# Performance work log

Measured on AMD Instinct MI355X. Metric: run time of the kernel, lower is better.

Reference implementation:

```python
import jax, jax.numpy as jnp
import numpy as np

N_USER = 250_000
N_ITEM = 250_000
E = 500_000
IN, H, C = 128, 64, 2
NEG_SLOPE = 0.01  # torch F.leaky_relu default


def setup_inputs() -> dict:
    key = jax.random.key(0)
    ks = jax.random.split(key, 24)
    d = {}
    d["feat_user"] = jax.random.normal(ks[0], (N_USER, IN), jnp.float32)
    d["feat_item"] = jax.random.normal(ks[1], (N_ITEM, IN), jnp.float32)
    # per-etype linear params, layer 1 (in_feats -> h_dim)
    s1 = 1.0 / np.sqrt(IN)
    d["W1_follows"] = jax.random.normal(ks[2], (IN, H), jnp.float32) * s1
    d["b1_follows"] = jax.random.normal(ks[3], (H,), jnp.float32) * s1
    d["W1_clicks"]  = jax.random.normal(ks[4], (IN, H), jnp.float32) * s1
    d["b1_clicks"]  = jax.random.normal(ks[5], (H,), jnp.float32) * s1
    d["W1_rev"]     = jax.random.normal(ks[6], (IN, H), jnp.float32) * s1
    d["b1_rev"]     = jax.random.normal(ks[7], (H,), jnp.float32) * s1
    # per-etype linear params, layer 2 (h_dim -> num_classes)
    s2 = 1.0 / np.sqrt(H)
    d["W2_follows"] = jax.random.normal(ks[8], (H, C), jnp.float32) * s2
    d["b2_follows"] = jax.random.normal(ks[9], (C,), jnp.float32) * s2
    d["W2_clicks"]  = jax.random.normal(ks[10], (H, C), jnp.float32) * s2
    d["b2_clicks"]  = jax.random.normal(ks[11], (C,), jnp.float32) * s2
    d["W2_rev"]     = jax.random.normal(ks[12], (H, C), jnp.float32) * s2
    d["b2_rev"]     = jax.random.normal(ks[13], (C,), jnp.float32) * s2
    # edge lists: (src, dst) per canonical etype
    d["follows_src"] = jax.random.randint(ks[14], (E,), 0, N_USER, jnp.int32)  # user->user
    d["follows_dst"] = jax.random.randint(ks[15], (E,), 0, N_USER, jnp.int32)
    d["clicks_src"]  = jax.random.randint(ks[16], (E,), 0, N_USER, jnp.int32)  # user->item
    d["clicks_dst"]  = jax.random.randint(ks[17], (E,), 0, N_ITEM, jnp.int32)
    d["rev_src"]     = jax.random.randint(ks[18], (E,), 0, N_ITEM, jnp.int32)  # item->user
    d["rev_dst"]     = jax.random.randint(ks[19], (E,), 0, N_USER, jnp.int32)
    return d


def _mean_agg(Wh, src, dst, n_dst):
    # copy_u + mean: gather transformed src feats per edge, segment-mean onto dst
    m = Wh[src]                                                   # [E, d]
    s = jax.ops.segment_sum(m, dst, num_segments=n_dst)           # [n_dst, d]
    deg = jax.ops.segment_sum(jnp.ones_like(dst, Wh.dtype), dst, num_segments=n_dst)
    return s / jnp.maximum(deg, 1.0)[:, None]                     # 0 for deg-0 nodes (DGL fills 0)


def _layer(fu, fi, Wf, bf, Wc, bc, Wr, br,
           fsrc, fdst, csrc, cdst, rsrc, rdst):
    # per-etype linear on src features, per-etype mean, cross-etype 'sum'
    h_user = (_mean_agg(fu @ Wf + bf, fsrc, fdst, N_USER)
              + _mean_agg(fi @ Wr + br, rsrc, rdst, N_USER))
    h_item = _mean_agg(fu @ Wc + bc, csrc, cdst, N_ITEM)
    return h_user, h_item


def reference(feat_user, feat_item,
              W1_follows, b1_follows, W1_clicks, b1_clicks, W1_rev, b1_rev,
              W2_follows, b2_follows, W2_clicks, b2_clicks, W2_rev, b2_rev,
              follows_src, follows_dst, clicks_src, clicks_dst, rev_src, rev_dst):
    h1u, h1i = _layer(feat_user, feat_item,
                      W1_follows, b1_follows, W1_clicks, b1_clicks, W1_rev, b1_rev,
                      follows_src, follows_dst, clicks_src, clicks_dst, rev_src, rev_dst)
    h2u = jnp.where(h1u >= 0, h1u, NEG_SLOPE * h1u)
    h2i = jnp.where(h1i >= 0, h1i, NEG_SLOPE * h1i)
    out_u, out_i = _layer(h2u, h2i,
                          W2_follows, b2_follows, W2_clicks, b2_clicks, W2_rev, b2_rev,
                          follows_src, follows_dst, clicks_src, clicks_dst, rev_src, rev_dst)
    # (h_dict, h_dict_2) flattened per ntype
    return (out_u, out_i, h2u, h2i)
```

## Files before the change

kernel.cpp:

```cpp
#include <hip/hip_runtime.h>
#include <cstdio>

#define NU 250000
#define NI 250000
#define NE 500000
#define ND 250000
#define NB_SCAN 245
#define NR 8
#define RSZ 31250

typedef __attribute__((ext_vector_type(8))) short short8v;
typedef __attribute__((ext_vector_type(4))) float float4v;

__device__ inline unsigned short f2bf(float x) {
  unsigned int b = __float_as_uint(x);
  unsigned int r = (b + 0x7FFFu + ((b >> 16) & 1u)) >> 16;
  return (unsigned short)r;
}
__device__ inline float bf2f(unsigned short u) {
  return __uint_as_float(((unsigned int)u) << 16);
}

__global__ void hist3_kernel(const int* __restrict__ fdst, const int* __restrict__ cdst,
                             const int* __restrict__ rdst,
                             int* __restrict__ degf, int* __restrict__ degc, int* __restrict__ degr) {
  int i = blockIdx.x * blockDim.x + threadIdx.x;
  if (i < NE) {
    atomicAdd(&degf[fdst[i]], 1);
    atomicAdd(&degc[cdst[i]], 1);
    atomicAdd(&degr[rdst[i]], 1);
  }
}

__global__ void scan1_kernel(const int* __restrict__ deg0, const int* __restrict__ deg1,
                             const int* __restrict__ deg2, int* __restrict__ bsum) {
  const int* deg = blockIdx.y == 0 ? deg0 : (blockIdx.y == 1 ? deg1 : deg2);
  int* bs = bsum + blockIdx.y * 256;
  __shared__ int s[256];
  int b = blockIdx.x, t = threadIdx.x;
  int base = b * 1024 + t * 4;
  int v = 0;
  #pragma unroll
  for (int i = 0; i < 4; ++i) if (base + i < ND) v += deg[base + i];
  s[t] = v; __syncthreads();
  for (int off = 128; off > 0; off >>= 1) { if (t < off) s[t] += s[t + off]; __syncthreads(); }
  if (t == 0) bs[b] = s[0];
}

__global__ void scan2_kernel(int* __restrict__ bsum) {
  int* bs = bsum + blockIdx.x * 256;
  __shared__ int s[256];
  int t = threadIdx.x;
  s[t] = (t < NB_SCAN) ? bs[t] : 0;
  __syncthreads();
  for (int off = 1; off < 256; off <<= 1) {
    int x = (t >= off) ? s[t - off] : 0;
    __syncthreads();
    s[t] += x;
    __syncthreads();
  }
  if (t < NB_SCAN) bs[t] = (t == 0) ? 0 : s[t - 1];
}

__global__ void scan3_kernel(const int* __restrict__ deg0, const int* __restrict__ deg1,
                             const int* __restrict__ deg2, const int* __restrict__ bsum,
                             int* __restrict__ offs0, int* __restrict__ offs1, int* __restrict__ offs2,
                             int* __restrict__ cur0, int* __restrict__ cur1, int* __restrict__ cur2) {
  int y = blockIdx.y;
  const int* deg = y == 0 ? deg0 : (y == 1 ? deg1 : deg2);
  int* offs = y == 0 ? offs0 : (y == 1 ? offs1 : offs2);
  int* cursor = y == 0 ? cur0 : (y == 1 ? cur1 : cur2);
  const int* bs = bsum + y * 256;
  __shared__ int s[256];
  int b = blockIdx.x, t = threadIdx.x;
  int base = b * 1024 + t * 4;
  int v[4]; int sum = 0;
  #pragma unroll
  for (int i = 0; i < 4; ++i) { v[i] = (base + i < ND) ? deg[base + i] : 0; sum += v[i]; }
  s[t] = sum; __syncthreads();
  for (int off = 1; off < 256; off <<= 1) {
    int x = (t >= off) ? s[t - off] : 0;
    __syncthreads();
    s[t] += x;
    __syncthreads();
  }
  int run = bs[b] + s[t] - sum;
  #pragma unroll
  for (int i = 0; i < 4; ++i) {
    if (base + i < ND) { offs[base + i] = run; cursor[base + i] = run; run += v[i]; }
  }
  if (b == 0 && t == 0) offs[ND] = NE;
}

__global__ void bucket_part_kernel(const int* __restrict__ fsrc, const int* __restrict__ fdst,
                                   const int* __restrict__ csrc, const int* __restrict__ cdst,
                                   const int* __restrict__ rsrc, const int* __restrict__ rdst,
                                   int* __restrict__ curf, int* __restrict__ curc, int* __restrict__ curr,
                                   int* __restrict__ srtf, int* __restrict__ srtc, int* __restrict__ srtr) {
  const int r = blockIdx.x & (NR - 1);
  const int chunk = blockIdx.x >> 3;
  const int lo = r * RSZ, hi = lo + RSZ;
  const int base = chunk * 1024;
  #pragma unroll
  for (int i = 0; i < 4; ++i) {
    int e = base + i * 256 + threadIdx.x;
    if (e < NE) {
      int d0 = fdst[e]; int s0 = fsrc[e];
      if (d0 >= lo && d0 < hi) { int p = atomicAdd(&curf[d0], 1); srtf[p] = s0; }
      int d1 = cdst[e]; int s1 = csrc[e];
      if (d1 >= lo && d1 < hi) { int p = atomicAdd(&curc[d1], 1); srtc[p] = s1; }
      int d2 = rdst[e]; int s2 = rsrc[e];
      if (d2 >= lo && d2 < hi) { int p = atomicAdd(&curr[d2], 1); srtr[p] = s2; }
    }
  }
}

__global__ void prepw_kernel(const float* __restrict__ W0, const float* __restrict__ W1,
                             const float* __restrict__ W2, unsigned short* __restrict__ T) {
  int gt = blockIdx.x * 256 + threadIdx.x;
  int et = gt >> 10;
  int g = gt & 1023;
  int gl = g & 63;
  int jm = (g >> 6) & 3;
  int c = g >> 8;
  int kb = c * 32 + (gl >> 4) * 8;
  int col = jm * 16 + (gl & 15);
  const float* W = et == 0 ? W0 : (et == 1 ? W1 : W2);
  short8v u;
  #pragma unroll
  for (int i = 0; i < 8; ++i) u[i] = (short)f2bf(W[(kb + i) * 64 + col]);
  ((short8v*)T)[gt] = u;
}

template <int NG, bool TWO>
__global__ __launch_bounds__(256) void gemm_kernel(
    const float* __restrict__ X, int n,
    const unsigned short* __restrict__ Ta, const float* __restrict__ ba,
    const unsigned short* __restrict__ Tb, const float* __restrict__ bb,
    unsigned short* __restrict__ Ya, unsigned short* __restrict__ Yb) {
  const int tid = threadIdx.x;
  const int lane = tid & 63;
  const int wave = tid >> 6;
  const int base = blockIdx.x * (NG * 64) + wave * (NG * 16);

  int node[NG];
  const float* xrow[NG];
  #pragma unroll
  for (int g = 0; g < NG; ++g) {
    node[g] = base + g * 16 + (lane & 15);
    int rowc = node[g] < n ? node[g] : (n - 1);
    xrow[g] = X + (size_t)rowc * 128 + (lane >> 4) * 8;
  }

  float4v accA[NG][4] = {};
  float4v accB[NG][4] = {};

  #pragma unroll
  for (int c = 0; c < 4; ++c) {
    short8v a[4], a2[4];
    #pragma unroll
    for (int jm = 0; jm < 4; ++jm) {
      a[jm] = ((const short8v*)Ta)[c * 256 + jm * 64 + lane];
      if constexpr (TWO) a2[jm] = ((const short8v*)Tb)[c * 256 + jm * 64 + lane];
    }
    #pragma unroll
    for (int g = 0; g < NG; ++g) {
      float4 f0 = *(const float4*)(xrow[g] + c * 32);
      float4 f1 = *(const float4*)(xrow[g] + c * 32 + 4);
      short8v bfr;
      bfr[0] = (short)f2bf(f0.x); bfr[1] = (short)f2bf(f0.y);
      bfr[2] = (short)f2bf(f0.z); bfr[3] = (short)f2bf(f0.w);
      bfr[4] = (short)f2bf(f1.x); bfr[5] = (short)f2bf(f1.y);
      bfr[6] = (short)f2bf(f1.z); bfr[7] = (short)f2bf(f1.w);
      #pragma unroll
      for (int jm = 0; jm < 4; ++jm) {
        accA[g][jm] = __builtin_amdgcn_mfma_f32_16x16x32_bf16(a[jm], bfr, accA[g][jm], 0, 0, 0);
        if constexpr (TWO)
          accB[g][jm] = __builtin_amdgcn_mfma_f32_16x16x32_bf16(a2[jm], bfr, accB[g][jm], 0, 0, 0);
      }
    }
  }

  const int cb = (lane >> 4) * 4;
  #pragma unroll
  for (int g = 0; g < NG; ++g) {
    if (node[g] < n) {
      #pragma unroll
      for (int jm = 0; jm < 4; ++jm) {
        float4 bias = *(const float4*)&ba[jm * 16 + cb];
        ushort4 o;
        o.x = f2bf(accA[g][jm][0] + bias.x);
        o.y = f2bf(accA[g][jm][1] + bias.y);
        o.z = f2bf(accA[g][jm][2] + bias.z);
        o.w = f2bf(accA[g][jm][3] + bias.w);
        *(ushort4*)&Ya[(size_t)node[g] * 64 + jm * 16 + cb] = o;
        if constexpr (TWO) {
          float4 bias2 = *(const float4*)&bb[jm * 16 + cb];
          ushort4 o2;
          o2.x = f2bf(accB[g][jm][0] + bias2.x);
          o2.y = f2bf(accB[g][jm][1] + bias2.y);
          o2.z = f2bf(accB[g][jm][2] + bias2.z);
          o2.w = f2bf(accB[g][jm][3] + bias2.w);
          *(ushort4*)&Yb[(size_t)node[g] * 64 + jm * 16 + cb] = o2;
        }
      }
    }
  }
}

__global__ __launch_bounds__(256) void agg_user_kernel(
    const unsigned short* __restrict__ Whf, const unsigned short* __restrict__ Whr,
    const int* __restrict__ offs_f, const int* __restrict__ srt_f,
    const int* __restrict__ offs_r, const int* __restrict__ srt_r,
    const float* __restrict__ W2f, const float* __restrict__ b2f,
    const float* __restrict__ W2c, const float* __restrict__ b2c,
    float* __restrict__ h2u, float* __restrict__ Y2f, float* __restrict__ Y2c) {
  int t = blockIdx.x * 256 + threadIdx.x;
  int d = t >> 4, q = t & 15;
  if (d >= NU) return;

  float af[4] = {0.f, 0.f, 0.f, 0.f};
  int f0 = offs_f[d], f1 = offs_f[d + 1];
  for (int e = f0; e < f1; ++e) {
    int s = srt_f[e];
    ushort4 v = *(const ushort4*)&Whf[(size_t)s * 64 + q * 4];
    af[0] += bf2f(v.x); af[1] += bf2f(v.y); af[2] += bf2f(v.z); af[3] += bf2f(v.w);
  }
  float rf = 1.0f / fmaxf((float)(f1 - f0), 1.0f);

  float ar[4] = {0.f, 0.f, 0.f, 0.f};
  int r0 = offs_r[d], r1 = offs_r[d + 1];
  for (int e = r0; e < r1; ++e) {
    int s = srt_r[e];
    ushort4 v = *(const ushort4*)&Whr[(size_t)s * 64 + q * 4];
    ar[0] += bf2f(v.x); ar[1] += bf2f(v.y); ar[2] += bf2f(v.z); ar[3] += bf2f(v.w);
  }
  float rr = 1.0f / fmaxf((float)(r1 - r0), 1.0f);

  float h[4];
  #pragma unroll
  for (int i = 0; i < 4; ++i) {
    float x = af[i] * rf + ar[i] * rr;
    h[i] = x >= 0.f ? x : 0.01f * x;
  }
  *(float4*)&h2u[(size_t)d * 64 + q * 4] = make_float4(h[0], h[1], h[2], h[3]);

  float pf0 = 0.f, pf1 = 0.f, pc0 = 0.f, pc1 = 0.f;
  #pragma unroll
  for (int i = 0; i < 4; ++i) {
    int j = q * 4 + i;
    pf0 += h[i] * W2f[j * 2 + 0]; pf1 += h[i] * W2f[j * 2 + 1];
    pc0 += h[i] * W2c[j * 2 + 0]; pc1 += h[i] * W2c[j * 2 + 1];
  }
  #pragma unroll
  for (int off = 1; off < 16; off <<= 1) {
    pf0 += __shfl_xor(pf0, off, 64);
    pf1 += __shfl_xor(pf1, off, 64);
    pc0 += __shfl_xor(pc0, off, 64);
    pc1 += __shfl_xor(pc1, off, 64);
  }
  if (q == 0) {
    Y2f[(size_t)d * 2 + 0] = pf0 + b2f[0];
    Y2f[(size_t)d * 2 + 1] = pf1 + b2f[1];
    Y2c[(size_t)d * 2 + 0] = pc0 + b2c[0];
    Y2c[(size_t)d * 2 + 1] = pc1 + b2c[1];
  }
}

__global__ __launch_bounds__(256) void agg_item_kernel(
    const unsigned short* __restrict__ Whc,
    const int* __restrict__ offs_c, const int* __restrict__ srt_c,
    const float* __restrict__ W2r, const float* __restrict__ b2r,
    float* __restrict__ h2i, float* __restrict__ Y2r) {
  int t = blockIdx.x * 256 + threadIdx.x;
  int d = t >> 4, q = t & 15;
  if (d >= NI) return;

  float ac[4] = {0.f, 0.f, 0.f, 0.f};
  int c0 = offs_c[d], c1 = offs_c[d + 1];
  for (int e = c0; e < c1; ++e) {
    int s = srt_c[e];
    ushort4 v = *(const ushort4*)&Whc[(size_t)s * 64 + q * 4];
    ac[0] += bf2f(v.x); ac[1] += bf2f(v.y); ac[2] += bf2f(v.z); ac[3] += bf2f(v.w);
  }
  float rc = 1.0f / fmaxf((float)(c1 - c0), 1.0f);

  float h[4];
  #pragma unroll
  for (int i = 0; i < 4; ++i) {
    float x = ac[i] * rc;
    h[i] = x >= 0.f ? x : 0.01f * x;
  }
  *(float4*)&h2i[(size_t)d * 64 + q * 4] = make_float4(h[0], h[1], h[2], h[3]);

  float p0 = 0.f, p1 = 0.f;
  #pragma unroll
  for (int i = 0; i < 4; ++i) {
    int j = q * 4 + i;
    p0 += h[i] * W2r[j * 2 + 0]; p1 += h[i] * W2r[j * 2 + 1];
  }
  #pragma unroll
  for (int off = 1; off < 16; off <<= 1) {
    p0 += __shfl_xor(p0, off, 64);
    p1 += __shfl_xor(p1, off, 64);
  }
  if (q == 0) {
    Y2r[(size_t)d * 2 + 0] = p0 + b2r[0];
    Y2r[(size_t)d * 2 + 1] = p1 + b2r[1];
  }
}

__global__ void out_user_kernel(const float* __restrict__ Y2f, const float* __restrict__ Y2r,
                                const int* __restrict__ offs_f, const int* __restrict__ srt_f,
                                const int* __restrict__ offs_r, const int* __restrict__ srt_r,
                                float* __restrict__ out_u) {
  int d = blockIdx.x * blockDim.x + threadIdx.x;
  if (d >= NU) return;
  int f0 = offs_f[d], f1 = offs_f[d + 1];
  float a0 = 0.f, a1 = 0.f;
  for (int e = f0; e < f1; ++e) {
    int s = srt_f[e];
    a0 += Y2f[(size_t)s * 2 + 0]; a1 += Y2f[(size_t)s * 2 + 1];
  }
  float rf = 1.0f / fmaxf((float)(f1 - f0), 1.0f);
  int r0 = offs_r[d], r1 = offs_r[d + 1];
  float c0 = 0.f, c1 = 0.f;
  for (int e = r0; e < r1; ++e) {
    int s = srt_r[e];
    c0 += Y2r[(size_t)s * 2 + 0]; c1 += Y2r[(size_t)s * 2 + 1];
  }
  float rr = 1.0f / fmaxf((float)(r1 - r0), 1.0f);
  out_u[(size_t)d * 2 + 0] = a0 * rf + c0 * rr;
  out_u[(size_t)d * 2 + 1] = a1 * rf + c1 * rr;
}

__global__ void out_item_kernel(const float* __restrict__ Y2c,
                                const int* __restrict__ offs_c, const int* __restrict__ srt_c,
                                float* __restrict__ out_i) {
  int d = blockIdx.x * blockDim.x + threadIdx.x;
  if (d >= NI) return;
  int c0o = offs_c[d], c1o = offs_c[d + 1];
  float a0 = 0.f, a1 = 0.f;
  for (int e = c0o; e < c1o; ++e) {
    int s = srt_c[e];
    a0 += Y2c[(size_t)s * 2 + 0]; a1 += Y2c[(size_t)s * 2 + 1];
  }
  float rc = 1.0f / fmaxf((float)(c1o - c0o), 1.0f);
  out_i[(size_t)d * 2 + 0] = a0 * rc;
  out_i[(size_t)d * 2 + 1] = a1 * rc;
}

extern "C" void kernel_launch(void* const* d_in, const int* in_sizes, int n_in,
                              void* d_out, int out_size, void* d_ws, size_t ws_size,
                              hipStream_t stream) {
  const float* feat_user = (const float*)d_in[0];
  const float* feat_item = (const float*)d_in[1];
  const float* W1f = (const float*)d_in[2];  const float* b1f = (const float*)d_in[3];
  const float* W1c = (const float*)d_in[4];  const float* b1c = (const float*)d_in[5];
  const float* W1r = (const float*)d_in[6];  const float* b1r = (const float*)d_in[7];
  const float* W2f = (const float*)d_in[8];  const float* b2f = (const float*)d_in[9];
  const float* W2c = (const float*)d_in[10]; const float* b2c = (const float*)d_in[11];
  const float* W2r = (const float*)d_in[12]; const float* b2r = (const float*)d_in[13];
  const int* fsrc = (const int*)d_in[14];  const int* fdst = (const int*)d_in[15];
  const int* csrc = (const int*)d_in[16];  const int* cdst = (const int*)d_in[17];
  const int* rsrc = (const int*)d_in[18];  const int* rdst = (const int*)d_in[19];

  float* out = (float*)d_out;
  float* out_u = out;
  float* out_i = out + 2 * NU;
  float* h2u  = out + 1000000;
  float* h2i  = out + 17000000;

  unsigned short* Whf = (unsigned short*)d_ws;
  unsigned short* Whc = Whf + 16000000;
  unsigned short* Whr = Whc + 16000000;
  unsigned short* Wtab = Whr + 16000000;
  unsigned short* Tf = Wtab;
  unsigned short* Tc = Wtab + 8192;
  unsigned short* Tr = Wtab + 16384;
  int* ibase = (int*)(Wtab + 24576);
  const int P = 250304;
  int* offs_f = ibase;            int* offs_c = offs_f + P;  int* offs_r = offs_c + P;
  int* cur_f  = offs_r + P;       int* cur_c  = cur_f + P;   int* cur_r  = cur_c + P;
  int* deg_f  = cur_r + P;        int* deg_c  = deg_f + P;   int* deg_r  = deg_c + P;
  int* srt_f  = deg_r + P;
  int* srt_c  = srt_f + 500096;
  int* srt_r  = srt_c + 500096;
  int* bsum   = srt_r + 500096;
  float* Y2f  = (float*)(bsum + 768);
  float* Y2c  = Y2f + 500000;
  float* Y2r  = Y2c + 500000;

  size_t need = 96000000ull + 24576ull * 2ull
              + (9ull * P + 3ull * 500096ull + 768ull + 1500000ull) * 4ull;
  if (ws_size < need) {
    fprintf(stderr, "kernel_launch: ws too small (%zu < %zu)\n", ws_size, need);
    return;
  }

  hipMemsetAsync(deg_f, 0, (size_t)(3 * P) * 4, stream);

  const int eb = (NE + 255) / 256;

  prepw_kernel<<<12, 256, 0, stream>>>(W1f, W1c, W1r, Wtab);

  gemm_kernel<2, true><<<(NU + 127) / 128, 256, 0, stream>>>(feat_user, NU, Tf, b1f, Tc, b1c, Whf, Whc);
  gemm_kernel<4, false><<<(NI + 255) / 256, 256, 0, stream>>>(feat_item, NI, Tr, b1r, nullptr, nullptr, Whr, nullptr);

  hist3_kernel<<<eb, 256, 0, stream>>>(fdst, cdst, rdst, deg_f, deg_c, deg_r);
  scan1_kernel<<<dim3(NB_SCAN, 3), 256, 0, stream>>>(deg_f, deg_c, deg_r, bsum);
  scan2_kernel<<<3, 256, 0, stream>>>(bsum);
  scan3_kernel<<<dim3(NB_SCAN, 3), 256, 0, stream>>>(deg_f, deg_c, deg_r, bsum,
                                                     offs_f, offs_c, offs_r,
                                                     cur_f, cur_c, cur_r);
  const int chunks = (NE + 1023) / 1024;
  bucket_part_kernel<<<chunks * NR, 256, 0, stream>>>(fsrc, fdst, csrc, cdst, rsrc, rdst,
                                                      cur_f, cur_c, cur_r, srt_f, srt_c, srt_r);

  const int ab = (NU * 16 + 255) / 256;
  agg_user_kernel<<<ab, 256, 0, stream>>>(Whf, Whr, offs_f, srt_f, offs_r, srt_r,
                                          W2f, b2f, W2c, b2c, h2u, Y2f, Y2c);
  agg_item_kernel<<<ab, 256, 0, stream>>>(Whc, offs_c, srt_c, W2r, b2r, h2i, Y2r);

  const int nb = (NU + 255) / 256;
  out_user_kernel<<<nb, 256, 0, stream>>>(Y2f, Y2r, offs_f, srt_f, offs_r, srt_r, out_u);
  out_item_kernel<<<nb, 256, 0, stream>>>(Y2c, offs_c, srt_c, out_i);
}
```

Baseline: 376.5 us.

## Stream GEMM input tiles through double-buffered LDS with async global-to-LDS copies

Replaces the one-shot layer-1 GEMM kernels with a persistent kernel of 512 blocks. Each block loops over 64-row tiles and prefetches the next tile into a double-buffered, XOR-swizzled LDS buffer using global_load_lds DMA while computing the current one. Weight fragments and biases are hoisted into registers once per block. The goal is to hide global load latency in this bandwidth-bound projection. In exchange it uses 64KB of LDS per block, which limits occupancy, and adds a barrier per tile.

```diff
diff --git a/kernel.cpp b/kernel.cpp
--- a/kernel.cpp
+++ b/kernel.cpp
@@ -19,6 +19,11 @@
 }
 __device__ inline float bf2f(unsigned short u) {
   return __uint_as_float(((unsigned int)u) << 16);
+}
+
+__device__ inline void async_copy16(const float* g, float* l) {
+  __builtin_amdgcn_global_load_lds((const __attribute__((address_space(1))) void*)g,
+                                   (__attribute__((address_space(3))) void*)l, 16, 0, 0);
 }
 
 __global__ void hist3_kernel(const int* __restrict__ fdst, const int* __restrict__ cdst,
@@ -132,41 +137,75 @@
   ((short8v*)T)[gt] = u;
 }
 
-template <int NG, bool TWO>
-__global__ __launch_bounds__(256) void gemm_kernel(
-    const float* __restrict__ X, int n,
+template <bool TWO>
+__global__ __launch_bounds__(256, 2) void gemm_dma_kernel(
+    const float* __restrict__ X, int n, int ntiles,
     const unsigned short* __restrict__ Ta, const float* __restrict__ ba,
     const unsigned short* __restrict__ Tb, const float* __restrict__ bb,
     unsigned short* __restrict__ Ya, unsigned short* __restrict__ Yb) {
+  __shared__ float sx[2][64 * 128];
   const int tid = threadIdx.x;
   const int lane = tid & 63;
   const int wave = tid >> 6;
-  const int base = blockIdx.x * (NG * 64) + wave * (NG * 16);
-
-  int node[NG];
-  const float* xrow[NG];
-  #pragma unroll
-  for (int g = 0; g < NG; ++g) {
-    node[g] = base + g * 16 + (lane & 15);
-    int rowc = node[g] < n ? node[g] : (n - 1);
-    xrow[g] = X + (size_t)rowc * 128 + (lane >> 4) * 8;
-  }
-
-  float4v accA[NG][4] = {};
-  float4v accB[NG][4] = {};
-
+  const int cb = (lane >> 4) * 4;
+
+  short8v A[4][4], B[4][4];
   #pragma unroll
   for (int c = 0; c < 4; ++c) {
-    short8v a[4], a2[4];
     #pragma unroll
     for (int jm = 0; jm < 4; ++jm) {
-      a[jm] = ((const short8v*)Ta)[c * 256 + jm * 64 + lane];
-      if constexpr (TWO) a2[jm] = ((const short8v*)Tb)[c * 256 + jm * 64 + lane];
-    }
+      A[c][jm] = ((const short8v*)Ta)[c * 256 + jm * 64 + lane];
+      if constexpr (TWO) B[c][jm] = ((const short8v*)Tb)[c * 256 + jm * 64 + lane];
+    }
+  }
+  float4 bias_a[4], bias_b[4];
+  #pragma unroll
+  for (int jm = 0; jm < 4; ++jm) {
+    bias_a[jm] = *(const float4*)&ba[jm * 16 + cb];
+    if constexpr (TWO) bias_b[jm] = *(const float4*)&bb[jm * 16 + cb];
+  }
+
+  const int nl = wave * 16 + (lane & 15);
+  const int sw = nl & 7;
+
+  int t = blockIdx.x;
+  {
     #pragma unroll
-    for (int g = 0; g < NG; ++g) {
-      float4 f0 = *(const float4*)(xrow[g] + c * 32);
-      float4 f1 = *(const float4*)(xrow[g] + c * 32 + 4);
+    for (int j = 0; j < 8; ++j) {
+      int idx = (wave * 8 + j) * 64 + lane;
+      int row = idx >> 5, u = idx & 31;
+      int gr = t * 64 + row; if (gr >= n) gr = n - 1;
+      const float* src = X + (size_t)gr * 128 + ((u ^ (row & 7)) << 2);
+      float* dst = &sx[0][(wave * 8 + j) * 256];
+      async_copy16(src, dst);
+    }
+  }
+  asm volatile("s_waitcnt vmcnt(0)" ::: "memory");
+  __syncthreads();
+
+  int cur = 0;
+  while (true) {
+    int tn = t + (int)gridDim.x;
+    bool more = (tn < ntiles);
+    if (more) {
+      #pragma unroll
+      for (int j = 0; j < 8; ++j) {
+        int idx = (wave * 8 + j) * 64 + lane;
+        int row = idx >> 5, u = idx & 31;
+        int gr = tn * 64 + row; if (gr >= n) gr = n - 1;
+        const float* src = X + (size_t)gr * 128 + ((u ^ (row & 7)) << 2);
+        float* dst = &sx[cur ^ 1][(wave * 8 + j) * 256];
+        async_copy16(src, dst);
+      }
+    }
+
+    float4v accA[4] = {};
+    float4v accB[4] = {};
+    #pragma unroll
+    for (int c = 0; c < 4; ++c) {
+      int s0 = c * 8 + (lane >> 4) * 2;
+      float4 f0 = *(const float4*)&sx[cur][nl * 128 + (((s0 + 0) ^ sw) << 2)];
+      float4 f1 = *(const float4*)&sx[cur][nl * 128 + (((s0 + 1) ^ sw) << 2)];
       short8v bfr;
       bfr[0] = (short)f2bf(f0.x); bfr[1] = (short)f2bf(f0.y);
       bfr[2] = (short)f2bf(f0.z); bfr[3] = (short)f2bf(f0.w);
@@ -174,37 +213,37 @@
       bfr[6] = (short)f2bf(f1.z); bfr[7] = (short)f2bf(f1.w);
       #pragma unroll
       for (int jm = 0; jm < 4; ++jm) {
-        accA[g][jm] = __builtin_amdgcn_mfma_f32_16x16x32_bf16(a[jm], bfr, accA[g][jm], 0, 0, 0);
+        accA[jm] = __builtin_amdgcn_mfma_f32_16x16x32_bf16(A[c][jm], bfr, accA[jm], 0, 0, 0);
         if constexpr (TWO)
-          accB[g][jm] = __builtin_amdgcn_mfma_f32_16x16x32_bf16(a2[jm], bfr, accB[g][jm], 0, 0, 0);
+          accB[jm] = __builtin_amdgcn_mfma_f32_16x16x32_bf16(B[c][jm], bfr, accB[jm], 0, 0, 0);
       }
     }
-  }
-
-  const int cb = (lane >> 4) * 4;
-  #pragma unroll
-  for (int g = 0; g < NG; ++g) {
-    if (node[g] < n) {
+    int node = t * 64 + nl;
+    if (node < n) {
       #pragma unroll
       for (int jm = 0; jm < 4; ++jm) {
-        float4 bias = *(const float4*)&ba[jm * 16 + cb];
         ushort4 o;
-        o.x = f2bf(accA[g][jm][0] + bias.x);
-        o.y = f2bf(accA[g][jm][1] + bias.y);
-        o.z = f2bf(accA[g][jm][2] + bias.z);
-        o.w = f2bf(accA[g][jm][3] + bias.w);
-        *(ushort4*)&Ya[(size_t)node[g] * 64 + jm * 16 + cb] = o;
+        o.x = f2bf(accA[jm][0] + bias_a[jm].x);
+        o.y = f2bf(accA[jm][1] + bias_a[jm].y);
+        o.z = f2bf(accA[jm][2] + bias_a[jm].z);
+        o.w = f2bf(accA[jm][3] + bias_a[jm].w);
+        *(ushort4*)&Ya[(size_t)node * 64 + jm * 16 + cb] = o;
         if constexpr (TWO) {
-          float4 bias2 = *(const float4*)&bb[jm * 16 + cb];
           ushort4 o2;
-          o2.x = f2bf(accB[g][jm][0] + bias2.x);
-          o2.y = f2bf(accB[g][jm][1] + bias2.y);
-          o2.z = f2bf(accB[g][jm][2] + bias2.z);
-          o2.w = f2bf(accB[g][jm][3] + bias2.w);
-          *(ushort4*)&Yb[(size_t)node[g] * 64 + jm * 16 + cb] = o2;
+          o2.x = f2bf(accB[jm][0] + bias_b[jm].x);
+          o2.y = f2bf(accB[jm][1] + bias_b[jm].y);
+          o2.z = f2bf(accB[jm][2] + bias_b[jm].z);
+          o2.w = f2bf(accB[jm][3] + bias_b[jm].w);
+          *(ushort4*)&Yb[(size_t)node * 64 + jm * 16 + cb] = o2;
         }
       }
     }
+
+    if (!more) break;
+    asm volatile("s_waitcnt vmcnt(0)" ::: "memory");
+    __syncthreads();
+    cur ^= 1;
+    t = tn;
   }
 }
 
@@ -404,8 +443,10 @@
 
   prepw_kernel<<<12, 256, 0, stream>>>(W1f, W1c, W1r, Wtab);
 
-  gemm_kernel<2, true><<<(NU + 127) / 128, 256, 0, stream>>>(feat_user, NU, Tf, b1f, Tc, b1c, Whf, Whc);
-  gemm_kernel<4, false><<<(NI + 255) / 256, 256, 0, stream>>>(feat_item, NI, Tr, b1r, nullptr, nullptr, Whr, nullptr);
+  const int utiles = (NU + 63) / 64;
+  const int itiles = (NI + 63) / 64;
+  gemm_dma_kernel<true><<<512, 256, 0, stream>>>(feat_user, NU, utiles, Tf, b1f, Tc, b1c, Whf, Whc);
+  gemm_dma_kernel<false><<<512, 256, 0, stream>>>(feat_item, NI, itiles, Tr, b1r, nullptr, nullptr, Whr, nullptr);
 
   hist3_kernel<<<eb, 256, 0, stream>>>(fdst, cdst, rdst, deg_f, deg_c, deg_r);
   scan1_kernel<<<dim3(NB_SCAN, 3), 256, 0, stream>>>(deg_f, deg_c, deg_r, bsum);
```

After: 353.6 us. 6.1% less time.
